# Performance work log

Measured on AMD Instinct MI355X. Metric: run time of the kernel, lower is better.

The kernel has to match this reference:

```python
import jax, jax.numpy as jnp
import numpy as np

B, D, OUT = 8192, 1024, 256
H1, H2 = 8, 4
EPS = 1e-5


def setup_inputs() -> dict:
    key = jax.random.key(0)
    ks = jax.random.split(key, 8)
    sc = lambda k, shape: jax.random.normal(k, shape, jnp.float32) * 0.05
    return {
        "x": jax.random.normal(ks[0], (B, D), jnp.float32),
        "W1": sc(ks[1], (D, H1, 1)),      # D diagonal blocks of the masked Linear(D -> 8D)
        "b1": sc(ks[2], (D * H1,)),
        "g1": jnp.ones((D * H1,), jnp.float32),
        "be1": jnp.zeros((D * H1,), jnp.float32),
        "W2": sc(ks[3], (D, H2, H1)),     # D diagonal blocks of the masked Linear(8D -> 4D)
        "b2": sc(ks[4], (D * H2,)),
        "g2": jnp.ones((D * H2,), jnp.float32),
        "be2": jnp.zeros((D * H2,), jnp.float32),
        "Wfc": sc(ks[5], (OUT, D * H2)),
        "bfc": sc(ks[6], (OUT,)),
    }


def _batchnorm(h, g, b):
    # BatchNorm1d in training mode: per-channel batch mean, biased variance
    mu = h.mean(axis=0)
    var = h.var(axis=0)  # ddof=0 (biased), matching torch normalization
    return g * (h - mu) * jax.lax.rsqrt(var + EPS) + b


def reference(x, W1, b1, g1, be1, W2, b2, g2, be2, Wfc, bfc):
    n = x.shape[0]
    # layer 1: per-feature (1 -> H1) block GEMM == masked dense Linear
    h = jnp.einsum("bdi,doi->bdo", x[:, :, None], W1).reshape(n, D * H1)
    h = jax.nn.relu(_batchnorm(h + b1, g1, be1))
    # layer 2: per-feature (H1 -> H2) block GEMM
    h = jnp.einsum("bdi,doi->bdo", h.reshape(n, D, H1), W2).reshape(n, D * H2)
    h = jax.nn.relu(_batchnorm(h + b2, g2, be2))
    # dense output head
    return h @ Wfc.T + bfc
```

## Files before the change

kernel.cpp:

```cpp
#include <hip/hip_runtime.h>

#define EPSV 1e-5f

typedef short bf16x8 __attribute__((ext_vector_type(8)));
typedef float f32x4 __attribute__((ext_vector_type(4)));

static __device__ __forceinline__ unsigned short f2b(float f) {
  union { float f; unsigned u; } v; v.f = f;
  return (unsigned short)((v.u + 0x7fffu + ((v.u >> 16) & 1u)) >> 16);
}

__global__ void k_pre(const float* __restrict__ wfc, unsigned short* __restrict__ wb,
                      const float* __restrict__ x, float* __restrict__ ps1) {
  if (blockIdx.x < 512) {
    const int f = blockIdx.x * 256 + threadIdx.x;
    const int l15 = f & 15, quad = (f >> 4) & 3, nb = (f >> 6) & 15, k32b = f >> 10;
    const int n = nb * 16 + l15;
    const int k = k32b * 32 + quad * 8;
    const float4* src = (const float4*)(wfc + (size_t)n * 4096 + k);
    float4 a = src[0], b = src[1];
    ushort4 o0, o1;
    o0.x = f2b(a.x); o0.y = f2b(a.y); o0.z = f2b(a.z); o0.w = f2b(a.w);
    o1.x = f2b(b.x); o1.y = f2b(b.y); o1.z = f2b(b.z); o1.w = f2b(b.w);
    *(ushort4*)(wb + (size_t)f * 8) = o0;
    *(ushort4*)(wb + (size_t)f * 8 + 4) = o1;
  } else {
    const int blk = blockIdx.x - 512;
    const int c = threadIdx.x * 4;
    const int r0 = blk * 32;
    float4 s = {0.f,0.f,0.f,0.f}, q = {0.f,0.f,0.f,0.f};
    for (int g = 0; g < 4; ++g) {
      float4 v[8];
#pragma unroll
      for (int j = 0; j < 8; ++j)
        v[j] = *(const float4*)(x + (size_t)(r0 + g*8 + j) * 1024 + c);
#pragma unroll
      for (int j = 0; j < 8; ++j) {
        s.x += v[j].x; s.y += v[j].y; s.z += v[j].z; s.w += v[j].w;
        q.x = fmaf(v[j].x, v[j].x, q.x); q.y = fmaf(v[j].y, v[j].y, q.y);
        q.z = fmaf(v[j].z, v[j].z, q.z); q.w = fmaf(v[j].w, v[j].w, q.w);
      }
    }
    *(float4*)(ps1 + (size_t)blk * 2048 + c) = s;
    *(float4*)(ps1 + (size_t)blk * 2048 + 1024 + c) = q;
  }
}

__global__ __launch_bounds__(256) void k_fin1(const float* __restrict__ ps1,
    const float* __restrict__ W1, const float* __restrict__ g1,
    const float* __restrict__ be1, float* __restrict__ pt) {
  __shared__ float redS[8][32], redQ[8][32];
  const int t = threadIdx.x;
  const int d0 = blockIdx.x * 32;
  const int dl = t & 31, slot = t >> 5;
  float s = 0.f, q = 0.f;
  for (int u = 0; u < 32; u += 8) {
#pragma unroll
    for (int w = 0; w < 8; ++w) {
      const size_t base = (size_t)(slot * 32 + u + w) * 2048 + d0 + dl;
      s += ps1[base];
      q += ps1[base + 1024];
    }
  }
  redS[slot][dl] = s; redQ[slot][dl] = q;
  __syncthreads();
  const int dloc = t >> 3, i = t & 7;
  float xs = 0.f, xq = 0.f;
#pragma unroll
  for (int p = 0; p < 8; ++p) { xs += redS[p][dloc]; xq += redQ[p][dloc]; }
  const float inv = 1.f / 8192.f;
  const int d = d0 + dloc;
  const int c = d * 8 + i;
  float mean = xs * inv;
  float var = xq * inv - mean * mean;
  float w = W1[c];
  float s1 = g1[c] * w * rsqrtf(w * w * var + EPSV);
  float t1 = be1[c] - s1 * mean;
  pt[i * 1024 + d] = s1;
  pt[(8 + i) * 1024 + d] = t1;
}

__global__ __launch_bounds__(256) void k_stats2(const float* __restrict__ x,
    const float* __restrict__ pt, const float* __restrict__ W2,
    float* __restrict__ ps2s, float* __restrict__ ps2q) {
  __shared__ float red[8][32][8];
  const int t = threadIdx.x;
  const int dl = t & 31, slot = t >> 5;
  const int d = blockIdx.x * 32 + dl;
  float s1v[8], t1v[8], w2v[32];
#pragma unroll
  for (int i = 0; i < 8; ++i) s1v[i] = pt[i * 1024 + d];
#pragma unroll
  for (int i = 0; i < 8; ++i) t1v[i] = pt[(8 + i) * 1024 + d];
  const float4* wp = (const float4*)(W2 + (size_t)d * 32);
#pragma unroll
  for (int i = 0; i < 8; ++i) {
    float4 v = wp[i];
    w2v[i*4+0]=v.x; w2v[i*4+1]=v.y; w2v[i*4+2]=v.z; w2v[i*4+3]=v.w;
  }
  float s[4] = {0.f,0.f,0.f,0.f}, q[4] = {0.f,0.f,0.f,0.f};
  const int b0 = blockIdx.y * 256 + slot * 32;
  for (int r = 0; r < 32; r += 8) {
    float xv[8];
#pragma unroll
    for (int j = 0; j < 8; ++j)
      xv[j] = x[(size_t)(b0 + r + j) * 1024 + d];
#pragma unroll
    for (int j = 0; j < 8; ++j) {
      float a1[8];
#pragma unroll
      for (int i = 0; i < 8; ++i) a1[i] = fmaxf(fmaf(s1v[i], xv[j], t1v[i]), 0.f);
#pragma unroll
      for (int o = 0; o < 4; ++o) {
        float h = 0.f;
#pragma unroll
        for (int i = 0; i < 8; ++i) h = fmaf(a1[i], w2v[o*8+i], h);
        s[o] += h;
        q[o] = fmaf(h, h, q[o]);
      }
    }
  }
#pragma unroll
  for (int j = 0; j < 4; ++j) {
    red[slot][dl][j] = s[j];
    red[slot][dl][4+j] = q[j];
  }
  __syncthreads();
  const int d2l = t >> 3, j = t & 7;
  float v = 0.f;
#pragma unroll
  for (int p = 0; p < 8; ++p) v += red[p][d2l][j];
  const int c2 = (blockIdx.x * 32 + d2l) * 4 + (t & 3);
  if (j < 4) ps2s[(size_t)blockIdx.y * 4096 + c2] = v;
  else       ps2q[(size_t)blockIdx.y * 4096 + c2] = v;
}

__global__ void k_fin2(const float* __restrict__ W2, const float* __restrict__ g2,
                       const float* __restrict__ be2, const float* __restrict__ ps2s,
                       const float* __restrict__ ps2q, float* __restrict__ pt) {
  const int c2 = blockIdx.x * 256 + threadIdx.x;
  const int d = c2 >> 2, o = c2 & 3;
  float sm = 0.f, sq = 0.f;
#pragma unroll
  for (int b = 0; b < 32; ++b) {
    sm += ps2s[(size_t)b * 4096 + c2];
    sq += ps2q[(size_t)b * 4096 + c2];
  }
  const float inv = 1.f / 8192.f;
  float m = sm * inv;
  float var = sq * inv - m * m;
  float s2 = g2[c2] * rsqrtf(var + EPSV);
  float t2 = be2[c2] - s2 * m;
  pt[(48 + o) * 1024 + d] = t2;
#pragma unroll
  for (int i = 0; i < 8; ++i)
    pt[(16 + o * 8 + i) * 1024 + d] = W2[(size_t)d * 32 + o * 8 + i] * s2;
}

__global__ __launch_bounds__(256, 2) void k_gemm(const float* __restrict__ x,
    const float* __restrict__ pt, const unsigned short* __restrict__ wb,
    const float* __restrict__ bfc, float* __restrict__ out) {
  __shared__ __align__(16) unsigned short As[64 * 136];
  const int t = threadIdx.x;
  const int lane = t & 63;
  const int wv = t >> 6;
  const int m0 = blockIdx.x * 64;
  const int kQ = blockIdx.y;
  const int d0 = kQ * 256;
  const int quad = lane >> 4;
  const int l15 = lane & 15;
  const int dl = t & 31, bs = t >> 5;
  const int chrot = (blockIdx.x & 1) << 2;

  f32x4 acc[4][4];
#pragma unroll
  for (int mt = 0; mt < 4; ++mt)
#pragma unroll
    for (int nt = 0; nt < 4; ++nt) {
      f32x4 z = {0.f, 0.f, 0.f, 0.f};
      acc[mt][nt] = z;
    }

  for (int chi = 0; chi < 8; ++chi) {
    const int ch = (chi + chrot) & 7;
    const int d = d0 + ch * 32 + dl;
    float pv[52];
#pragma unroll
    for (int i = 0; i < 52; ++i) pv[i] = pt[i * 1024 + d];
    __syncthreads();
#pragma unroll
    for (int r = 0; r < 8; ++r) {
      const int bl = bs * 8 + r;
      float xv = x[(size_t)(m0 + bl) * 1024 + d];
      float a1[8];
#pragma unroll
      for (int i = 0; i < 8; ++i) a1[i] = fmaxf(fmaf(pv[i], xv, pv[8+i]), 0.f);
      unsigned short o4[4];
#pragma unroll
      for (int o = 0; o < 4; ++o) {
        float h = pv[48 + o];
#pragma unroll
        for (int i = 0; i < 8; ++i) h = fmaf(a1[i], pv[16 + o*8 + i], h);
        o4[o] = f2b(fmaxf(h, 0.f));
      }
      *(ushort4*)&As[bl * 136 + dl * 4] = make_ushort4(o4[0], o4[1], o4[2], o4[3]);
    }
    __syncthreads();
#pragma unroll
    for (int kk = 0; kk < 4; ++kk) {
      bf16x8 af[4];
#pragma unroll
      for (int mt = 0; mt < 4; ++mt)
        af[mt] = *(const bf16x8*)&As[(mt*16 + l15) * 136 + kk*32 + quad*8];
      const int k32b = kQ * 32 + ch * 4 + kk;
#pragma unroll
      for (int nt = 0; nt < 4; ++nt) {
        const int frag = k32b * 16 + wv * 4 + nt;
        bf16x8 bfr = *(const bf16x8*)&wb[((size_t)frag * 64 + lane) * 8];
#pragma unroll
        for (int mt = 0; mt < 4; ++mt)
          acc[mt][nt] = __builtin_amdgcn_mfma_f32_16x16x32_bf16(af[mt], bfr,
                                                                acc[mt][nt], 0, 0, 0);
      }
    }
  }
#pragma unroll
  for (int nt = 0; nt < 4; ++nt) {
    const int col = wv * 64 + nt * 16 + l15;
    const float bias = (kQ == 0) ? bfc[col] : 0.f;
#pragma unroll
    for (int mt = 0; mt < 4; ++mt) {
#pragma unroll
      for (int r = 0; r < 4; ++r) {
        const int row = m0 + mt * 16 + quad * 4 + r;
        atomicAdd(&out[(size_t)row * 256 + col], acc[mt][nt][r] + bias);
      }
    }
  }
}

extern "C" void kernel_launch(void* const* d_in, const int* in_sizes, int n_in,
                              void* d_out, int out_size, void* d_ws, size_t ws_size,
                              hipStream_t stream) {
  const float* x   = (const float*)d_in[0];
  const float* W1  = (const float*)d_in[1];
  const float* g1  = (const float*)d_in[3];
  const float* be1 = (const float*)d_in[4];
  const float* W2  = (const float*)d_in[5];
  const float* g2  = (const float*)d_in[7];
  const float* be2 = (const float*)d_in[8];
  const float* Wfc = (const float*)d_in[9];
  const float* bfc = (const float*)d_in[10];
  float* out = (float*)d_out;

  char* ws = (char*)d_ws;
  unsigned short* wb = (unsigned short*)ws;
  float* pt     = (float*)(ws + (2u << 20));
  float* shared = (float*)(ws + (2u << 20) + (256u << 10));
  float* ps1  = shared;
  float* ps2s = shared;
  float* ps2q = shared + 32 * 4096;

  hipMemsetAsync(d_out, 0, (size_t)out_size * sizeof(float), stream);

  k_pre   <<<dim3(768),    256, 0, stream>>>(Wfc, wb, x, ps1);
  k_fin1  <<<dim3(32),     256, 0, stream>>>(ps1, W1, g1, be1, pt);
  k_stats2<<<dim3(32, 32), 256, 0, stream>>>(x, pt, W2, ps2s, ps2q);
  k_fin2  <<<dim3(16),     256, 0, stream>>>(W2, g2, be2, ps2s, ps2q, pt);
  k_gemm  <<<dim3(128, 4), 256, 0, stream>>>(x, pt, wb, bfc, out);
}
```

Baseline: 185.5 us.

## Double-buffer GEMM A-tile generation and shrink M tile for more occupancy

The per-feature parameter table changes from channel-major to feature-major (56 floats per feature), so each thread loads its 52 parameters as vectorized 16-byte loads instead of strided scalar loads. The GEMM kernel now uses 32-row M tiles with twice the blocks and higher launch bounds. It also double-buffers the shared A tile, prefetching the next chunk's parameters and x while running MFMAs on the current one. This is meant to overlap tile generation with matrix math and raise occupancy, at the cost of more atomic adds to the output and more register pressure from the prefetched values.

New measurement: 189.1 us. About the same (+1.9%).

```diff
diff --git a/kernel.cpp b/kernel.cpp
--- a/kernel.cpp
+++ b/kernel.cpp
@@ -76,8 +76,8 @@
   float w = W1[c];
   float s1 = g1[c] * w * rsqrtf(w * w * var + EPSV);
   float t1 = be1[c] - s1 * mean;
-  pt[i * 1024 + d] = s1;
-  pt[(8 + i) * 1024 + d] = t1;
+  pt[(size_t)d * 56 + i] = s1;
+  pt[(size_t)d * 56 + 8 + i] = t1;
 }
 
 __global__ __launch_bounds__(256) void k_stats2(const float* __restrict__ x,
@@ -88,10 +88,15 @@
   const int dl = t & 31, slot = t >> 5;
   const int d = blockIdx.x * 32 + dl;
   float s1v[8], t1v[8], w2v[32];
-#pragma unroll
-  for (int i = 0; i < 8; ++i) s1v[i] = pt[i * 1024 + d];
-#pragma unroll
-  for (int i = 0; i < 8; ++i) t1v[i] = pt[(8 + i) * 1024 + d];
+  {
+    const f32x4* pq = (const f32x4*)(pt + (size_t)d * 56);
+    f32x4 a = pq[0], b = pq[1], c = pq[2], e = pq[3];
+#pragma unroll
+    for (int j = 0; j < 4; ++j) {
+      s1v[j] = a[j]; s1v[4 + j] = b[j];
+      t1v[j] = c[j]; t1v[4 + j] = e[j];
+    }
+  }
   const float4* wp = (const float4*)(W2 + (size_t)d * 32);
 #pragma unroll
   for (int i = 0; i < 8; ++i) {
@@ -151,85 +156,114 @@
   float var = sq * inv - m * m;
   float s2 = g2[c2] * rsqrtf(var + EPSV);
   float t2 = be2[c2] - s2 * m;
-  pt[(48 + o) * 1024 + d] = t2;
+  pt[(size_t)d * 56 + 48 + o] = t2;
 #pragma unroll
   for (int i = 0; i < 8; ++i)
-    pt[(16 + o * 8 + i) * 1024 + d] = W2[(size_t)d * 32 + o * 8 + i] * s2;
-}
-
-__global__ __launch_bounds__(256, 2) void k_gemm(const float* __restrict__ x,
+    pt[(size_t)d * 56 + 16 + o * 8 + i] = W2[(size_t)d * 32 + o * 8 + i] * s2;
+}
+
+__global__ __launch_bounds__(256, 4) void k_gemm(const float* __restrict__ x,
     const float* __restrict__ pt, const unsigned short* __restrict__ wb,
     const float* __restrict__ bfc, float* __restrict__ out) {
-  __shared__ __align__(16) unsigned short As[64 * 136];
+  __shared__ __align__(16) unsigned short As[2][32 * 136];
   const int t = threadIdx.x;
   const int lane = t & 63;
   const int wv = t >> 6;
-  const int m0 = blockIdx.x * 64;
+  const int m0 = blockIdx.x * 32;
   const int kQ = blockIdx.y;
   const int d0 = kQ * 256;
   const int quad = lane >> 4;
   const int l15 = lane & 15;
   const int dl = t & 31, bs = t >> 5;
-  const int chrot = (blockIdx.x & 1) << 2;
-
-  f32x4 acc[4][4];
-#pragma unroll
-  for (int mt = 0; mt < 4; ++mt)
+  const int chrot = blockIdx.x & 7;
+
+  f32x4 acc[2][4];
+#pragma unroll
+  for (int mt = 0; mt < 2; ++mt)
 #pragma unroll
     for (int nt = 0; nt < 4; ++nt) {
       f32x4 z = {0.f, 0.f, 0.f, 0.f};
       acc[mt][nt] = z;
     }
 
+  float pv[52];
+  float xv[4];
+
+#define PREFETCH(CH) do {                                                   \
+    const int d_ = d0 + (CH) * 32 + dl;                                     \
+    const f32x4* pp_ = (const f32x4*)(pt + (size_t)d_ * 56);                \
+    _Pragma("unroll")                                                       \
+    for (int i_ = 0; i_ < 13; ++i_) {                                       \
+      f32x4 v_ = pp_[i_];                                                   \
+      pv[i_*4+0] = v_[0]; pv[i_*4+1] = v_[1];                               \
+      pv[i_*4+2] = v_[2]; pv[i_*4+3] = v_[3];                               \
+    }                                                                       \
+    _Pragma("unroll")                                                       \
+    for (int r_ = 0; r_ < 4; ++r_)                                          \
+      xv[r_] = x[(size_t)(m0 + bs * 4 + r_) * 1024 + d_];                   \
+  } while (0)
+
+#define GEN_TILE(NB) do {                                                   \
+    _Pragma("unroll")                                                       \
+    for (int r_ = 0; r_ < 4; ++r_) {                                        \
+      const float xvv_ = xv[r_];                                            \
+      float a1_[8];                                                         \
+      _Pragma("unroll")                                                     \
+      for (int i_ = 0; i_ < 8; ++i_)                                        \
+        a1_[i_] = fmaxf(fmaf(pv[i_], xvv_, pv[8 + i_]), 0.f);               \
+      unsigned short o4_[4];                                                \
+      _Pragma("unroll")                                                     \
+      for (int o_ = 0; o_ < 4; ++o_) {                                      \
+        float h_ = pv[48 + o_];                                             \
+        _Pragma("unroll")                                                   \
+        for (int i_ = 0; i_ < 8; ++i_)                                      \
+          h_ = fmaf(a1_[i_], pv[16 + o_ * 8 + i_], h_);                     \
+        o4_[o_] = f2b(fmaxf(h_, 0.f));                                      \
+      }                                                                     \
+      *(ushort4*)&As[NB][(bs * 4 + r_) * 136 + dl * 4] =                    \
+          make_ushort4(o4_[0], o4_[1], o4_[2], o4_[3]);                     \
+    }                                                                       \
+  } while (0)
+
+  PREFETCH(chrot);
+  GEN_TILE(0);
+  __syncthreads();
+
   for (int chi = 0; chi < 8; ++chi) {
+    const int cur = chi & 1;
     const int ch = (chi + chrot) & 7;
-    const int d = d0 + ch * 32 + dl;
-    float pv[52];
-#pragma unroll
-    for (int i = 0; i < 52; ++i) pv[i] = pt[i * 1024 + d];
-    __syncthreads();
-#pragma unroll
-    for (int r = 0; r < 8; ++r) {
-      const int bl = bs * 8 + r;
-      float xv = x[(size_t)(m0 + bl) * 1024 + d];
-      float a1[8];
-#pragma unroll
-      for (int i = 0; i < 8; ++i) a1[i] = fmaxf(fmaf(pv[i], xv, pv[8+i]), 0.f);
-      unsigned short o4[4];
-#pragma unroll
-      for (int o = 0; o < 4; ++o) {
-        float h = pv[48 + o];
-#pragma unroll
-        for (int i = 0; i < 8; ++i) h = fmaf(a1[i], pv[16 + o*8 + i], h);
-        o4[o] = f2b(fmaxf(h, 0.f));
-      }
-      *(ushort4*)&As[bl * 136 + dl * 4] = make_ushort4(o4[0], o4[1], o4[2], o4[3]);
-    }
-    __syncthreads();
+    if (chi + 1 < 8) {
+      const int chn = (chi + 1 + chrot) & 7;
+      PREFETCH(chn);
+    }
 #pragma unroll
     for (int kk = 0; kk < 4; ++kk) {
-      bf16x8 af[4];
-#pragma unroll
-      for (int mt = 0; mt < 4; ++mt)
-        af[mt] = *(const bf16x8*)&As[(mt*16 + l15) * 136 + kk*32 + quad*8];
+      bf16x8 af0 = *(const bf16x8*)&As[cur][l15 * 136 + kk * 32 + quad * 8];
+      bf16x8 af1 = *(const bf16x8*)&As[cur][(16 + l15) * 136 + kk * 32 + quad * 8];
       const int k32b = kQ * 32 + ch * 4 + kk;
 #pragma unroll
       for (int nt = 0; nt < 4; ++nt) {
         const int frag = k32b * 16 + wv * 4 + nt;
         bf16x8 bfr = *(const bf16x8*)&wb[((size_t)frag * 64 + lane) * 8];
-#pragma unroll
-        for (int mt = 0; mt < 4; ++mt)
-          acc[mt][nt] = __builtin_amdgcn_mfma_f32_16x16x32_bf16(af[mt], bfr,
-                                                                acc[mt][nt], 0, 0, 0);
+        acc[0][nt] = __builtin_amdgcn_mfma_f32_16x16x32_bf16(af0, bfr, acc[0][nt], 0, 0, 0);
+        acc[1][nt] = __builtin_amdgcn_mfma_f32_16x16x32_bf16(af1, bfr, acc[1][nt], 0, 0, 0);
       }
     }
-  }
+    if (chi + 1 < 8) {
+      GEN_TILE(cur ^ 1);
+    }
+    __syncthreads();
+  }
+
+#undef PREFETCH
+#undef GEN_TILE
+
 #pragma unroll
   for (int nt = 0; nt < 4; ++nt) {
     const int col = wv * 64 + nt * 16 + l15;
     const float bias = (kQ == 0) ? bfc[col] : 0.f;
 #pragma unroll
-    for (int mt = 0; mt < 4; ++mt) {
+    for (int mt = 0; mt < 2; ++mt) {
 #pragma unroll
       for (int r = 0; r < 4; ++r) {
         const int row = m0 + mt * 16 + quad * 4 + r;
@@ -267,5 +301,5 @@
   k_fin1  <<<dim3(32),     256, 0, stream>>>(ps1, W1, g1, be1, pt);
   k_stats2<<<dim3(32, 32), 256, 0, stream>>>(x, pt, W2, ps2s, ps2q);
   k_fin2  <<<dim3(16),     256, 0, stream>>>(W2, g2, be2, ps2s, ps2q, pt);
-  k_gemm  <<<dim3(128, 4), 256, 0, stream>>>(x, pt, wb, bfc, out);
-}
+  k_gemm  <<<dim3(256, 4), 256, 0, stream>>>(x, pt, wb, bfc, out);
+}
```
